# Kernel tuning notes

Measured on AMD Instinct MI355X. Metric: run time of the kernel, lower is better.

## Reference

```python
import jax, jax.numpy as jnp
import numpy as np

EPS = 1e-8

def _qparams(x, bits):
    # AsymmetricSignedQParams + GlobalMinMaxObserver: per-tensor min/max,
    # signed range [-2^(b-1), 2^(b-1)-1], asymmetric zero point.
    qmin = -(2 ** (bits - 1))
    qmax = 2 ** (bits - 1) - 1
    mn = jnp.minimum(jnp.min(x), 0.0)
    mx = jnp.maximum(jnp.max(x), 0.0)
    scale = jnp.maximum((mx - mn) / (qmax - qmin), EPS)
    zp = jnp.clip(jnp.round(qmin - mn / scale), qmin, qmax)
    return scale, zp, qmin, qmax

def _fake_quant(x, bits):
    # quantize -> clamp -> dequantize (simulated fixed-point as in float forward)
    scale, zp, qmin, qmax = _qparams(x, bits)
    q = jnp.clip(jnp.round(x / scale) + zp, qmin, qmax)
    return (q - zp) * scale


def setup_inputs() -> dict:
    key = jax.random.key(0)
    k1, k2, k3 = jax.random.split(key, 3)
    B, W, H, D = 8, 1024, 8, 64
    q = jax.random.normal(k1, (B, W, H, D), dtype=jnp.float32)
    k = jax.random.normal(k2, (B, W, H, D), dtype=jnp.float32)
    v = jax.random.normal(k3, (B, W, H, D), dtype=jnp.float32)
    return {"q": q, "k": k, "v": v, "quant_bits": 8}


def reference(q, k, v, quant_bits):
    bits = int(quant_bits)
    d_model = q.shape[-1]
    inv_sqrt_d = 1.0 / np.sqrt(d_model)

    # quantize-dequantize inputs (inputs_{q,k,v}_QParams)
    qf = _fake_quant(q, bits)
    kf = _fake_quant(k, bits)
    vf = _fake_quant(v, bits)

    # matrix_multi_score: quantized QK^T with folded 1/sqrt(d) scale,
    # then requantize output (matrix_multi_score.outputs_QParams)
    scores = jnp.einsum("bqhd,bkhd->bhqk", qf, kf) * inv_sqrt_d
    scores = _fake_quant(scores, bits)

    # SoftmaxLUT: softmax over last dim, result requantized (softmax.outputs_QParams)
    att = jax.nn.softmax(scores, axis=-1)
    att_q = _fake_quant(att, bits)

    # matrix_multi_att: quantized att @ V, requantized output
    context = jnp.einsum("bhqk,bkhd->bqhd", att_q, vf)
    context = _fake_quant(context, bits)

    return context, att_q
```

## Files before the change

### kernel.cpp

```cpp
#include <hip/hip_runtime.h>
#include <cstdint>
#include <cstddef>

#define W  1024
#define NH 8
#define NB 8
#define DH 64
#define BHN (NB*NH)
#define CTX_ELEMS ((size_t)NB*W*NH*DH)
#define NS 64
#define ROWF 512
#define L2E 1.4426950408889634f

typedef int v4i __attribute__((ext_vector_type(4)));


__device__ __forceinline__ unsigned enc_f(float f){
  unsigned u = __float_as_uint(f);
  return (u & 0x80000000u) ? ~u : (u | 0x80000000u);
}
__device__ __forceinline__ float dec_f(unsigned k){
  unsigned u = (k & 0x80000000u) ? (k ^ 0x80000000u) : ~k;
  return __uint_as_float(u);
}

__device__ __forceinline__ float fq1(float x, float s, float z, float mn, float mx){
  float t = rintf(x / s) + z;
  t = fminf(fmaxf(t, mn), mx);
  return (t - z) * s;
}
__device__ __forceinline__ int qint_m(float x, float is, float z, float mn, float mx){
  return (int)fminf(fmaxf(rintf(x * is) + z, mn), mx);
}
__device__ __forceinline__ unsigned pack4(int a0, int a1, int a2, int a3){
  return (unsigned)(a0 & 0xff) | ((unsigned)(a1 & 0xff) << 8) |
         ((unsigned)(a2 & 0xff) << 16) | ((unsigned)(a3 & 0xff) << 24);
}

__device__ __forceinline__ unsigned* slot_min(unsigned* s, int t){ return s + (size_t)(2*t)*NS; }
__device__ __forceinline__ unsigned* slot_max(unsigned* s, int t){ return s + (size_t)(2*t+1)*NS; }

struct QP { float s, z; };

__device__ __forceinline__ QP qp_generic(const unsigned* slots, int t, float qmn, float qmx){
  const unsigned* pm = slots + (size_t)(2*t)*NS;
  const unsigned* px = pm + NS;
  unsigned em = pm[0], ex = px[0];
  for (int i = 1; i < NS; ++i){
    unsigned a = pm[i], b = px[i];
    em = (a < em) ? a : em;
    ex = (b > ex) ? b : ex;
  }
  float mn = dec_f(em), mx = dec_f(ex);
  QP r;
  r.s = fmaxf((mx - mn) / (qmx - qmn), 1e-8f);
  r.z = fminf(fmaxf(rintf(qmn - mn / r.s), qmn), qmx);
  return r;
}
__device__ __forceinline__ QP qp_scores(const int* jmn, const int* jmx, float sq, float sk,
                                        float qmn, float qmx){
  int em = jmn[0], ex = jmx[0];
  for (int i = 1; i < NS; ++i){ em = min(em, jmn[i]); ex = max(ex, jmx[i]); }
  float cfac = 0.125f * (sq * sk);
  float mn = fminf(cfac * (float)em, 0.0f);
  float mx = fmaxf(cfac * (float)ex, 0.0f);
  QP r;
  r.s = fmaxf((mx - mn) / (qmx - qmn), 1e-8f);
  r.z = fminf(fmaxf(rintf(qmn - mn / r.s), qmn), qmx);
  return r;
}

__device__ __forceinline__ void blk_minmax_atomic(float lmin, float lmax,
                                                  unsigned* smin, unsigned* smax){
  #pragma unroll
  for (int o = 32; o; o >>= 1){
    lmin = fminf(lmin, __shfl_xor(lmin, o));
    lmax = fmaxf(lmax, __shfl_xor(lmax, o));
  }
  __shared__ float wmn[4], wmx[4];
  int wid = threadIdx.x >> 6, lane = threadIdx.x & 63;
  if (lane == 0){ wmn[wid] = lmin; wmx[wid] = lmax; }
  __syncthreads();
  if (threadIdx.x == 0){
    float a = wmn[0], b = wmx[0];
    for (int w = 1; w < (int)(blockDim.x >> 6); ++w){
      a = fminf(a, wmn[w]); b = fmaxf(b, wmx[w]);
    }
    atomicMin(smin, enc_f(a));
    atomicMax(smax, enc_f(b));
  }
}

__device__ __forceinline__ void blk_iminmax_atomic(int lmin, int lmax, int* gmin, int* gmax){
  #pragma unroll
  for (int o = 32; o; o >>= 1){
    lmin = min(lmin, __shfl_xor(lmin, o));
    lmax = max(lmax, __shfl_xor(lmax, o));
  }
  __shared__ int iwmn[4], iwmx[4];
  int wid = threadIdx.x >> 6, lane = threadIdx.x & 63;
  if (lane == 0){ iwmn[wid] = lmin; iwmx[wid] = lmax; }
  __syncthreads();
  if (threadIdx.x == 0){
    int a = iwmn[0], b = iwmx[0];
    for (int w = 1; w < (int)(blockDim.x >> 6); ++w){
      a = min(a, iwmn[w]); b = max(b, iwmx[w]);
    }
    atomicMin(gmin, a);
    atomicMax(gmax, b);
  }
}

__device__ __forceinline__ void stage_tile(const float* __restrict__ rowptr,
                                           signed char (*S)[80], int* __restrict__ Ssum,
                                           float is, float z, float mn, float mx, int t){
  const int rr = t >> 2, dq = (t & 3) << 4;
  const float* p = rowptr + (size_t)rr * ROWF + dq;
  int part = 0;
  #pragma unroll
  for (int g = 0; g < 4; ++g){
    float4 x = *(const float4*)(p + g * 4);
    int a0 = qint_m(x.x, is, z, mn, mx), a1 = qint_m(x.y, is, z, mn, mx);
    int a2 = qint_m(x.z, is, z, mn, mx), a3 = qint_m(x.w, is, z, mn, mx);
    part += a0 + a1 + a2 + a3;
    *(unsigned*)&S[rr][dq + g*4] = pack4(a0, a1, a2, a3);
  }
  int x1 = part + __shfl_xor(part, 1);
  int tot = x1 + __shfl_xor(x1, 2);
  if ((t & 3) == 0) Ssum[rr] = tot;
}

__device__ __forceinline__ v4i qfrag_direct(const float* __restrict__ qrow, int lg,
                                            float is, float z, float mn, float mx,
                                            int* sqi_out){
  const float* p = qrow + (lg << 4);
  int part = 0; unsigned d4[4];
  #pragma unroll
  for (int g = 0; g < 4; ++g){
    float4 x = *(const float4*)(p + g * 4);
    int a0 = qint_m(x.x, is, z, mn, mx), a1 = qint_m(x.y, is, z, mn, mx);
    int a2 = qint_m(x.z, is, z, mn, mx), a3 = qint_m(x.w, is, z, mn, mx);
    part += a0 + a1 + a2 + a3;
    d4[g] = pack4(a0, a1, a2, a3);
  }
  part += __shfl_xor(part, 16);
  part += __shfl_xor(part, 32);
  *sqi_out = part;
  v4i r; r[0] = (int)d4[0]; r[1] = (int)d4[1]; r[2] = (int)d4[2]; r[3] = (int)d4[3];
  return r;
}


__global__ void init_slots_kernel(unsigned* __restrict__ slots, int* __restrict__ jmn,
                                  int* __restrict__ jmx, int* __restrict__ Sv8){
  for (int i = threadIdx.x; i < 6*2*NS; i += blockDim.x)
    slots[i] = 0x80000000u;
  if (threadIdx.x < NS){
    jmn[threadIdx.x] = 0x7fffffff;
    jmx[threadIdx.x] = (int)0x80000000;
  }
  for (int i = threadIdx.x; i < BHN*64; i += blockDim.x) Sv8[i] = 0;
}

__global__ __launch_bounds__(256) void minmax3_kernel(const float* __restrict__ q,
                                                      const float* __restrict__ k,
                                                      const float* __restrict__ v,
                                                      unsigned* __restrict__ slots){
  const float4* p = (const float4*)(blockIdx.y == 0 ? q : (blockIdx.y == 1 ? k : v));
  float lmin = 0.f, lmax = 0.f;
  const int n4 = (int)(CTX_ELEMS / 4);
  for (int i = blockIdx.x * blockDim.x + threadIdx.x; i < n4; i += gridDim.x * blockDim.x){
    float4 x = p[i];
    lmin = fminf(lmin, fminf(fminf(x.x, x.y), fminf(x.z, x.w)));
    lmax = fmaxf(lmax, fmaxf(fmaxf(x.x, x.y), fmaxf(x.z, x.w)));
  }
  const int idx = blockIdx.x & (NS - 1);
  blk_minmax_atomic(lmin, lmax, slot_min(slots, blockIdx.y) + idx, slot_max(slots, blockIdx.y) + idx);
}


__global__ __launch_bounds__(256) void pass1a_kernel(const float* __restrict__ kg,
                                                     const float* __restrict__ vg,
                                                     const unsigned* __restrict__ slots,
                                                     const int* __restrict__ bits_p,
                                                     char* __restrict__ k8,
                                                     int* __restrict__ Sk8,
                                                     char* __restrict__ v8,
                                                     int* __restrict__ Sv8){
  __shared__ int ColS[64];
  const int bits = *bits_p;
  const float qmx = (float)((1 << (bits-1)) - 1), qmn = -(float)(1 << (bits-1));
  const QP kp = qp_generic(slots, 1, qmn, qmx);
  const QP vp = qp_generic(slots, 2, qmn, qmx);
  const int it = blockIdx.x, bh = blockIdx.y, b = bh >> 3, h = bh & 7;
  const int i0 = it << 6, t = threadIdx.x;

  {
    const int rr = t >> 2, dq = (t & 3) << 4;
    const float* p = kg + ((size_t)(b*W + i0 + rr) * NH + h) * DH + dq;
    const float isk = 1.0f / kp.s;
    int part = 0; unsigned d4[4];
    #pragma unroll
    for (int g = 0; g < 4; ++g){
      float4 x = *(const float4*)(p + g * 4);
      int a0 = qint_m(x.x, isk, kp.z, qmn, qmx), a1 = qint_m(x.y, isk, kp.z, qmn, qmx);
      int a2 = qint_m(x.z, isk, kp.z, qmn, qmx), a3 = qint_m(x.w, isk, kp.z, qmn, qmx);
      part += a0 + a1 + a2 + a3;
      d4[g] = pack4(a0, a1, a2, a3);
    }
    uint4 u; u.x = d4[0]; u.y = d4[1]; u.z = d4[2]; u.w = d4[3];
    *(uint4*)(k8 + ((size_t)bh << 16) + (((size_t)(i0 + rr)) << 6) + dq) = u;
    int x1 = part + __shfl_xor(part, 1);
    int tot = x1 + __shfl_xor(x1, 2);
    if ((t & 3) == 0) Sk8[(bh << 10) + i0 + rr] = tot;
  }

  {
    const int dq4 = (t & 15) << 2, kb = (t >> 4) << 2;
    const float* vp_ = vg + ((size_t)(b*W + i0 + kb) * NH + h) * DH + dq4;
    const float isv = 1.0f / vp.s;
    float4 x0 = *(const float4*)(vp_);
    float4 x1 = *(const float4*)(vp_ + ROWF);
    float4 x2 = *(const float4*)(vp_ + 2 * ROWF);
    float4 x3 = *(const float4*)(vp_ + 3 * ROWF);
    int q00 = qint_m(x0.x, isv, vp.z, qmn, qmx), q01 = qint_m(x0.y, isv, vp.z, qmn, qmx),
        q02 = qint_m(x0.z, isv, vp.z, qmn, qmx), q03 = qint_m(x0.w, isv, vp.z, qmn, qmx);
    int q10 = qint_m(x1.x, isv, vp.z, qmn, qmx), q11 = qint_m(x1.y, isv, vp.z, qmn, qmx),
        q12 = qint_m(x1.z, isv, vp.z, qmn, qmx), q13 = qint_m(x1.w, isv, vp.z, qmn, qmx);
    int q20 = qint_m(x2.x, isv, vp.z, qmn, qmx), q21 = qint_m(x2.y, isv, vp.z, qmn, qmx),
        q22 = qint_m(x2.z, isv, vp.z, qmn, qmx), q23 = qint_m(x2.w, isv, vp.z, qmn, qmx);
    int q30 = qint_m(x3.x, isv, vp.z, qmn, qmx), q31 = qint_m(x3.y, isv, vp.z, qmn, qmx),
        q32 = qint_m(x3.z, isv, vp.z, qmn, qmx), q33 = qint_m(x3.w, isv, vp.z, qmn, qmx);
    unsigned w0 = pack4(q00, q10, q20, q30);
    unsigned w1 = pack4(q01, q11, q21, q31);
    unsigned w2 = pack4(q02, q12, q22, q32);
    unsigned w3 = pack4(q03, q13, q23, q33);
    char* vb = v8 + ((size_t)bh << 16) + i0 + kb;
    *(unsigned*)(vb + ((size_t)(dq4 + 0) << 10)) = w0;
    *(unsigned*)(vb + ((size_t)(dq4 + 1) << 10)) = w1;
    *(unsigned*)(vb + ((size_t)(dq4 + 2) << 10)) = w2;
    *(unsigned*)(vb + ((size_t)(dq4 + 3) << 10)) = w3;
    int cv0 = q00 + q10 + q20 + q30;
    int cv1 = q01 + q11 + q21 + q31;
    int cv2 = q02 + q12 + q22 + q32;
    int cv3 = q03 + q13 + q23 + q33;
    if (t < 64) ColS[t] = 0;
    __syncthreads();
    atomicAdd(&ColS[dq4 + 0], cv0);
    atomicAdd(&ColS[dq4 + 1], cv1);
    atomicAdd(&ColS[dq4 + 2], cv2);
    atomicAdd(&ColS[dq4 + 3], cv3);
    __syncthreads();
    if (t < 64) atomicAdd(&Sv8[(bh << 6) + t], ColS[t]);
  }
}

__global__ __launch_bounds__(256) void pass1b_kernel(const float* __restrict__ qg,
                                                     const unsigned* __restrict__ slots,
                                                     const int* __restrict__ bits_p,
                                                     float* __restrict__ stash,
                                                     int* __restrict__ jmn,
                                                     int* __restrict__ jmx,
                                                     const char* __restrict__ k8,
                                                     const int* __restrict__ Sk8){
  const int bits = *bits_p;
  const float qmx = (float)((1 << (bits-1)) - 1), qmn = -(float)(1 << (bits-1));
  const QP qq = qp_generic(slots, 0, qmn, qmx);
  const QP kp = qp_generic(slots, 1, qmn, qmx);
  const int it = blockIdx.x, bh = blockIdx.y, b = bh >> 3, h = bh & 7;
  const int i0 = it << 6, t = threadIdx.x;
  const int lane = t & 63, w = t >> 6, lr = lane & 15, lg = lane >> 4;
  const int irow = (w << 4) + lr;
  const int izq = (int)qq.z, izk = (int)kp.z, c64 = 64 * izq * izk;

  int sqi;
  v4i Bq = qfrag_direct(qg + ((size_t)(b*W + i0 + irow) * NH + h) * DH, lg,
                        1.0f / qq.s, qq.z, qmn, qmx, &sqi);
  const char* kb = k8 + ((size_t)bh << 16);
  const int* skb = Sk8 + (bh << 10);

  int gmin = 0x7fffffff, gmax = (int)0x80000000, rmax = (int)0x80000000;
  for (int cc = 0; cc < 16; ++cc){
    #pragma unroll
    for (int jt = 0; jt < 4; ++jt){
      v4i Ak = *(const v4i*)(kb + (((size_t)((cc << 6) + (jt << 4) + lr)) << 6) + (lg << 4));
      v4i s4 = *(const v4i*)(skb + (cc << 6) + (jt << 4) + (lg << 2));
      v4i zz = {0, 0, 0, 0};
      v4i acc = __builtin_amdgcn_mfma_i32_16x16x64_i8(Ak, Bq, zz, 0, 0, 0);
      #pragma unroll
      for (int r = 0; r < 4; ++r){
        int J = acc[r] - izq * s4[r] - izk * sqi + c64;
        gmin = min(gmin, J); gmax = max(gmax, J); rmax = max(rmax, J);
      }
    }
  }
  rmax = max(rmax, __shfl_xor(rmax, 16));
  rmax = max(rmax, __shfl_xor(rmax, 32));
  if (lg == 0)
    stash[((size_t)(b*W + i0 + irow) * NH + h) * DH] = __int_as_float(rmax);
  const int idx = (it + bh * 16) & (NS - 1);
  blk_iminmax_atomic(gmin, gmax, jmn + idx, jmx + idx);
}

__global__ __launch_bounds__(256) void pass2c_kernel(const float* __restrict__ qg,
                                                     unsigned* __restrict__ slots,
                                                     const int* __restrict__ jmn,
                                                     const int* __restrict__ jmx,
                                                     const int* __restrict__ bits_p,
                                                     float* __restrict__ stash,
                                                     const char* __restrict__ k8,
                                                     const int* __restrict__ Sk8){
  const int bits = *bits_p;
  const float qmx = (float)((1 << (bits-1)) - 1), qmn = -(float)(1 << (bits-1));
  const QP qq = qp_generic(slots, 0, qmn, qmx);
  const QP kp = qp_generic(slots, 1, qmn, qmx);
  const QP sp = qp_scores(jmn, jmx, qq.s, kp.s, qmn, qmx);
  const int it = blockIdx.x, bh = blockIdx.y, b = bh >> 3, h = bh & 7;
  const int i0 = it << 6, t = threadIdx.x;
  const int lane = t & 63, w = t >> 6, lr = lane & 15, lg = lane >> 4;
  const int irow = (w << 4) + lr;
  const int izq = (int)qq.z, izk = (int)kp.z, c64 = 64 * izq * izk;
  const float rf = (0.125f * (qq.s * kp.s)) / sp.s;
  const float c2 = sp.s * L2E, zs = sp.z;

  int sqi;
  v4i Bq = qfrag_direct(qg + ((size_t)(b*W + i0 + irow) * NH + h) * DH, lg,
                        1.0f / qq.s, qq.z, qmn, qmx, &sqi);
  int Jm = __float_as_int(stash[((size_t)(b*W + i0 + irow) * NH + h) * DH]);
  const float tmxf = fminf(fmaxf(rintf((float)Jm * rf) + zs, qmn), qmx);
  const char* kb = k8 + ((size_t)bh << 16);
  const int* skb = Sk8 + (bh << 10);

  float zacc = 0.f;
  for (int cc = 0; cc < 16; ++cc){
    #pragma unroll
    for (int jt = 0; jt < 4; ++jt){
      v4i Ak = *(const v4i*)(kb + (((size_t)((cc << 6) + (jt << 4) + lr)) << 6) + (lg << 4));
      v4i s4 = *(const v4i*)(skb + (cc << 6) + (jt << 4) + (lg << 2));
      v4i zz = {0, 0, 0, 0};
      v4i acc = __builtin_amdgcn_mfma_i32_16x16x64_i8(Ak, Bq, zz, 0, 0, 0);
      int J0 = acc[0] - izq * s4[0] - izk * sqi + c64;
      int J1 = acc[1] - izq * s4[1] - izk * sqi + c64;
      int J2 = acc[2] - izq * s4[2] - izk * sqi + c64;
      int J3 = acc[3] - izq * s4[3] - izk * sqi + c64;
      float tl0 = fminf(fmaxf(rintf((float)J0 * rf) + zs, qmn), qmx);
      float tl1 = fminf(fmaxf(rintf((float)J1 * rf) + zs, qmn), qmx);
      float tl2 = fminf(fmaxf(rintf((float)J2 * rf) + zs, qmn), qmx);
      float tl3 = fminf(fmaxf(rintf((float)J3 * rf) + zs, qmn), qmx);
      zacc += exp2f((tl0 - tmxf) * c2);
      zacc += exp2f((tl1 - tmxf) * c2);
      zacc += exp2f((tl2 - tmxf) * c2);
      zacc += exp2f((tl3 - tmxf) * c2);
    }
  }
  zacc += __shfl_xor(zacc, 16);
  zacc += __shfl_xor(zacc, 32);
  if (lg == 0)
    stash[((size_t)(b*W + i0 + irow) * NH + h) * DH + 1] = zacc;
  float ratt = 1.0f / zacc;
  #pragma unroll
  for (int o = 1; o < 16; o <<= 1) ratt = fmaxf(ratt, __shfl_xor(ratt, o));
  if (lane == 0){
    const int idx = ((it << 2) + w + bh * 64) & (NS - 1);
    atomicMax(slot_max(slots, 4) + idx, enc_f(ratt));
  }
}

__global__ __launch_bounds__(256) void pass3c_kernel(const float* __restrict__ qg,
                                                     float* __restrict__ att,
                                                     float* __restrict__ ctx,
                                                     unsigned* __restrict__ slots,
                                                     const int* __restrict__ jmn,
                                                     const int* __restrict__ jmx,
                                                     const int* __restrict__ bits_p,
                                                     const char* __restrict__ k8,
                                                     const int* __restrict__ Sk8,
                                                     const char* __restrict__ v8,
                                                     const int* __restrict__ Sv8){
  __shared__ __align__(16) signed char As[64][80];
  __shared__ int RowA[64];
  const int bits = *bits_p;
  const float qmx = (float)((1 << (bits-1)) - 1), qmn = -(float)(1 << (bits-1));
  const QP qq = qp_generic(slots, 0, qmn, qmx);
  const QP kp = qp_generic(slots, 1, qmn, qmx);
  const QP sp = qp_scores(jmn, jmx, qq.s, kp.s, qmn, qmx);
  const QP vp = qp_generic(slots, 2, qmn, qmx);
  const QP ap = qp_generic(slots, 4, qmn, qmx);
  const int it = blockIdx.x, bh = blockIdx.y, b = bh >> 3, h = bh & 7;
  const int i0 = it << 6, t = threadIdx.x;
  const int lane = t & 63, w = t >> 6, lr = lane & 15, lg = lane >> 4;
  const int irow = (w << 4) + lr;
  const int izq = (int)qq.z, izk = (int)kp.z, c64 = 64 * izq * izk;
  const int iza = (int)ap.z, izv = (int)vp.z;
  const float rf = (0.125f * (qq.s * kp.s)) / sp.s;
  const float c2 = sp.s * L2E, zs = sp.z;
  const float sa = ap.s, za = ap.z, inv_sa = 1.0f / sa;

  int sqi;
  v4i Bq = qfrag_direct(qg + ((size_t)(b*W + i0 + irow) * NH + h) * DH, lg,
                        1.0f / qq.s, qq.z, qmn, qmx, &sqi);
  const size_t rbase = ((size_t)(b*W + i0 + irow) * NH + h) * DH;
  int Jm = __float_as_int(ctx[rbase]);
  const float tmxf = fminf(fmaxf(rintf((float)Jm * rf) + zs, qmn), qmx);
  const float iZ = 1.0f / ctx[rbase + 1];
  const char* kb = k8 + ((size_t)bh << 16);
  const int* skb = Sk8 + (bh << 10);
  const char* vb = v8 + ((size_t)bh << 16);

  int rA = 0;
  v4i accPV[4];
  #pragma unroll
  for (int tj = 0; tj < 4; ++tj){ v4i zz = {0,0,0,0}; accPV[tj] = zz; }

  for (int cc = 0; cc < 16; ++cc){
    #pragma unroll
    for (int jt = 0; jt < 4; ++jt){
      v4i Ak = *(const v4i*)(kb + (((size_t)((cc << 6) + (jt << 4) + lr)) << 6) + (lg << 4));
      v4i s4 = *(const v4i*)(skb + (cc << 6) + (jt << 4) + (lg << 2));
      v4i zz = {0, 0, 0, 0};
      v4i acc = __builtin_amdgcn_mfma_i32_16x16x64_i8(Ak, Bq, zz, 0, 0, 0);
      int J0 = acc[0] - izq * s4[0] - izk * sqi + c64;
      int J1 = acc[1] - izq * s4[1] - izk * sqi + c64;
      int J2 = acc[2] - izq * s4[2] - izk * sqi + c64;
      int J3 = acc[3] - izq * s4[3] - izk * sqi + c64;
      float tl0 = fminf(fmaxf(rintf((float)J0 * rf) + zs, qmn), qmx);
      float tl1 = fminf(fmaxf(rintf((float)J1 * rf) + zs, qmn), qmx);
      float tl2 = fminf(fmaxf(rintf((float)J2 * rf) + zs, qmn), qmx);
      float tl3 = fminf(fmaxf(rintf((float)J3 * rf) + zs, qmn), qmx);
      float p0 = exp2f((tl0 - tmxf) * c2) * iZ;
      float p1 = exp2f((tl1 - tmxf) * c2) * iZ;
      float p2 = exp2f((tl2 - tmxf) * c2) * iZ;
      float p3 = exp2f((tl3 - tmxf) * c2) * iZ;
      float a0 = fminf(fmaxf(rintf(p0 * inv_sa) + za, qmn), qmx);
      float a1 = fminf(fmaxf(rintf(p1 * inv_sa) + za, qmn), qmx);
      float a2 = fminf(fmaxf(rintf(p2 * inv_sa) + za, qmn), qmx);
      float a3 = fminf(fmaxf(rintf(p3 * inv_sa) + za, qmn), qmx);
      float4 y;
      y.x = (a0 - za) * sa; y.y = (a1 - za) * sa;
      y.z = (a2 - za) * sa; y.w = (a3 - za) * sa;
      *(float4*)(att + ((size_t)bh << 20) + (size_t)(i0 + irow) * W
                 + (cc << 6) + (jt << 4) + (lg << 2)) = y;
      int q0 = (int)a0, q1 = (int)a1, q2 = (int)a2, q3 = (int)a3;
      rA += q0 + q1 + q2 + q3;
      *(unsigned*)&As[irow][(jt << 4) + (lg << 2)] = pack4(q0, q1, q2, q3);
    }
    {
      v4i A2 = *(const v4i*)&As[(w << 4) + lr][lg << 4];
      #pragma unroll
      for (int tj = 0; tj < 4; ++tj){
        v4i B2 = *(const v4i*)(vb + (((size_t)((tj << 4) + lr)) << 10) + (cc << 6) + (lg << 4));
        accPV[tj] = __builtin_amdgcn_mfma_i32_16x16x64_i8(A2, B2, accPV[tj], 0, 0, 0);
      }
    }
  }

  rA += __shfl_xor(rA, 16);
  rA += __shfl_xor(rA, 32);
  if (lg == 0) RowA[irow] = rA;

  const float sav = sa * vp.s;
  float lmin = 0.f, lmax = 0.f;
  #pragma unroll
  for (int tj = 0; tj < 4; ++tj){
    const int d = (tj << 4) + lr;
    const int cvd = Sv8[(bh << 6) + d];
    #pragma unroll
    for (int r = 0; r < 4; ++r){
      const int i = (w << 4) + (lg << 2) + r;
      int Jv = accPV[tj][r] - iza * cvd - izv * RowA[i] + 1024 * iza * izv;
      float c = sav * (float)Jv;
      lmin = fminf(lmin, c); lmax = fmaxf(lmax, c);
      ctx[(((size_t)(b * W + i0 + i)) * NH + h) * DH + d] = c;
    }
  }
  const int idx = (it + bh * 16) & (NS - 1);
  blk_minmax_atomic(lmin, lmax, slot_min(slots, 5) + idx, slot_max(slots, 5) + idx);
}


__global__ __launch_bounds__(256) void pass1_plain(const float* __restrict__ qg,
                                                   const float* __restrict__ kg,
                                                   const unsigned* __restrict__ slots,
                                                   const int* __restrict__ bits_p,
                                                   float* __restrict__ stash,
                                                   int* __restrict__ jmn,
                                                   int* __restrict__ jmx){
  __shared__ __align__(16) signed char Qs[64][80], Ks[64][80];
  __shared__ int Sq[64], Sk[64];
  const int bits = *bits_p;
  const float qmx = (float)((1 << (bits-1)) - 1), qmn = -(float)(1 << (bits-1));
  const QP qq = qp_generic(slots, 0, qmn, qmx);
  const QP kp = qp_generic(slots, 1, qmn, qmx);
  const int it = blockIdx.x, bh = blockIdx.y, b = bh >> 3, h = bh & 7;
  const int i0 = it << 6, t = threadIdx.x;
  const int lane = t & 63, w = t >> 6, lr = lane & 15, lg = lane >> 4;
  const float isq = 1.0f / qq.s, isk = 1.0f / kp.s;
  const int izq = (int)qq.z, izk = (int)kp.z, c64 = 64 * izq * izk;

  stage_tile(qg + ((size_t)(b*W + i0) * NH + h) * DH, Qs, Sq, isq, qq.z, qmn, qmx, t);
  __syncthreads();
  const v4i Bq = *(const v4i*)&Qs[(w << 4) + lr][lg << 4];
  const int sqi = Sq[(w << 4) + lr];

  int gmin = 0x7fffffff, gmax = (int)0x80000000, rmax = (int)0x80000000;
  for (int cc = 0; cc < 16; ++cc){
    __syncthreads();
    stage_tile(kg + ((size_t)(b*W + (cc << 6)) * NH + h) * DH, Ks, Sk, isk, kp.z, qmn, qmx, t);
    __syncthreads();
    #pragma unroll
    for (int jt = 0; jt < 4; ++jt){
      v4i Ak = *(const v4i*)&Ks[(jt << 4) + lr][lg << 4];
      v4i zz = {0, 0, 0, 0};
      v4i acc = __builtin_amdgcn_mfma_i32_16x16x64_i8(Ak, Bq, zz, 0, 0, 0);
      v4i s4 = *(const v4i*)&Sk[(jt << 4) + (lg << 2)];
      #pragma unroll
      for (int r = 0; r < 4; ++r){
        int J = acc[r] - izq * s4[r] - izk * sqi + c64;
        gmin = min(gmin, J); gmax = max(gmax, J); rmax = max(rmax, J);
      }
    }
  }
  rmax = max(rmax, __shfl_xor(rmax, 16));
  rmax = max(rmax, __shfl_xor(rmax, 32));
  if (lg == 0)
    stash[((size_t)(b*W + i0 + (w << 4) + lr) * NH + h) * DH] = __int_as_float(rmax);
  const int idx = (it + bh * 16) & (NS - 1);
  blk_iminmax_atomic(gmin, gmax, jmn + idx, jmx + idx);
}

__global__ __launch_bounds__(256) void pass2_plain(const float* __restrict__ qg,
                                                   const float* __restrict__ kg,
                                                   unsigned* __restrict__ slots,
                                                   const int* __restrict__ jmn,
                                                   const int* __restrict__ jmx,
                                                   const int* __restrict__ bits_p,
                                                   float* __restrict__ stash){
  __shared__ __align__(16) signed char Qs[64][80], Ks[64][80];
  __shared__ int Sq[64], Sk[64];
  const int bits = *bits_p;
  const float qmx = (float)((1 << (bits-1)) - 1), qmn = -(float)(1 << (bits-1));
  const QP qq = qp_generic(slots, 0, qmn, qmx);
  const QP kp = qp_generic(slots, 1, qmn, qmx);
  const QP sp = qp_scores(jmn, jmx, qq.s, kp.s, qmn, qmx);
  const int it = blockIdx.x, bh = blockIdx.y, b = bh >> 3, h = bh & 7;
  const int i0 = it << 6, t = threadIdx.x;
  const int lane = t & 63, w = t >> 6, lr = lane & 15, lg = lane >> 4;
  const float isq = 1.0f / qq.s, isk = 1.0f / kp.s;
  const int izq = (int)qq.z, izk = (int)kp.z, c64 = 64 * izq * izk;
  const float rf = (0.125f * (qq.s * kp.s)) / sp.s;
  const float c2 = sp.s * L2E, zs = sp.z;
  const int irow = (w << 4) + lr;

  stage_tile(qg + ((size_t)(b*W + i0) * NH + h) * DH, Qs, Sq, isq, qq.z, qmn, qmx, t);
  __syncthreads();
  const v4i Bq = *(const v4i*)&Qs[irow][lg << 4];
  const int sqi = Sq[irow];
  int Jm = __float_as_int(stash[((size_t)(b*W + i0 + irow) * NH + h) * DH]);
  const float tmxf = fminf(fmaxf(rintf((float)Jm * rf) + zs, qmn), qmx);

  float zacc = 0.f;
  for (int cc = 0; cc < 16; ++cc){
    __syncthreads();
    stage_tile(kg + ((size_t)(b*W + (cc << 6)) * NH + h) * DH, Ks, Sk, isk, kp.z, qmn, qmx, t);
    __syncthreads();
    #pragma unroll
    for (int jt = 0; jt < 4; ++jt){
      v4i Ak = *(const v4i*)&Ks[(jt << 4) + lr][lg << 4];
      v4i zz = {0, 0, 0, 0};
      v4i acc = __builtin_amdgcn_mfma_i32_16x16x64_i8(Ak, Bq, zz, 0, 0, 0);
      v4i s4 = *(const v4i*)&Sk[(jt << 4) + (lg << 2)];
      int J0 = acc[0] - izq * s4[0] - izk * sqi + c64;
      int J1 = acc[1] - izq * s4[1] - izk * sqi + c64;
      int J2 = acc[2] - izq * s4[2] - izk * sqi + c64;
      int J3 = acc[3] - izq * s4[3] - izk * sqi + c64;
      float tl0 = fminf(fmaxf(rintf((float)J0 * rf) + zs, qmn), qmx);
      float tl1 = fminf(fmaxf(rintf((float)J1 * rf) + zs, qmn), qmx);
      float tl2 = fminf(fmaxf(rintf((float)J2 * rf) + zs, qmn), qmx);
      float tl3 = fminf(fmaxf(rintf((float)J3 * rf) + zs, qmn), qmx);
      zacc += exp2f((tl0 - tmxf) * c2);
      zacc += exp2f((tl1 - tmxf) * c2);
      zacc += exp2f((tl2 - tmxf) * c2);
      zacc += exp2f((tl3 - tmxf) * c2);
    }
  }
  zacc += __shfl_xor(zacc, 16);
  zacc += __shfl_xor(zacc, 32);
  if (lg == 0)
    stash[((size_t)(b*W + i0 + irow) * NH + h) * DH + 1] = zacc;
  float ratt = 1.0f / zacc;
  #pragma unroll
  for (int o = 1; o < 16; o <<= 1) ratt = fmaxf(ratt, __shfl_xor(ratt, o));
  if (lane == 0){
    const int idx = ((it << 2) + w + bh * 64) & (NS - 1);
    atomicMax(slot_max(slots, 4) + idx, enc_f(ratt));
  }
}

__global__ __launch_bounds__(256) void pass3_plain(const float* __restrict__ qg,
                                                   const float* __restrict__ kg,
                                                   const float* __restrict__ vg,
                                                   float* __restrict__ att,
                                                   float* __restrict__ ctx,
                                                   unsigned* __restrict__ slots,
                                                   const int* __restrict__ jmn,
                                                   const int* __restrict__ jmx,
                                                   const int* __restrict__ bits_p){
  __shared__ __align__(16) signed char Qs[64][80], Ks[64][80], Vs[64][80], As[64][80];
  __shared__ int Sq[64], Sk[64];
  __shared__ int RowA[64], ColV[64];
  const int bits = *bits_p;
  const float qmx = (float)((1 << (bits-1)) - 1), qmn = -(float)(1 << (bits-1));
  const QP qq = qp_generic(slots, 0, qmn, qmx);
  const QP kp = qp_generic(slots, 1, qmn, qmx);
  const QP sp = qp_scores(jmn, jmx, qq.s, kp.s, qmn, qmx);
  const QP vp = qp_generic(slots, 2, qmn, qmx);
  const QP ap = qp_generic(slots, 4, qmn, qmx);
  const int it = blockIdx.x, bh = blockIdx.y, b = bh >> 3, h = bh & 7;
  const int i0 = it << 6, t = threadIdx.x;
  const int lane = t & 63, w = t >> 6, lr = lane & 15, lg = lane >> 4;
  const float isq = 1.0f / qq.s, isk = 1.0f / kp.s;
  const int izq = (int)qq.z, izk = (int)kp.z, c64 = 64 * izq * izk;
  const float rf = (0.125f * (qq.s * kp.s)) / sp.s;
  const float c2 = sp.s * L2E, zs = sp.z;
  const float sa = ap.s, za = ap.z, inv_sa = 1.0f / sa;
  const float sv = vp.s, zv = vp.z, isv = 1.0f / sv;
  const int iza = (int)za, izv = (int)zv;
  const int irow = (w << 4) + lr;

  if (t < 64) ColV[t] = 0;
  stage_tile(qg + ((size_t)(b*W + i0) * NH + h) * DH, Qs, Sq, isq, qq.z, qmn, qmx, t);
  __syncthreads();
  const v4i Bq = *(const v4i*)&Qs[irow][lg << 4];
  const int sqi = Sq[irow];
  const size_t rbase = ((size_t)(b*W + i0 + irow) * NH + h) * DH;
  int Jm = __float_as_int(ctx[rbase]);
  const float tmxf = fminf(fmaxf(rintf((float)Jm * rf) + zs, qmn), qmx);
  const float iZ = 1.0f / ctx[rbase + 1];

  const int dq4 = (t & 15) << 2;
  const int kb  = (t >> 4) << 2;
  int cv4[4] = {0, 0, 0, 0};
  int rA = 0;
  v4i accPV[4];
  #pragma unroll
  for (int tj = 0; tj < 4; ++tj){ v4i zz = {0,0,0,0}; accPV[tj] = zz; }

  for (int cc = 0; cc < 16; ++cc){
    __syncthreads();
    stage_tile(kg + ((size_t)(b*W + (cc << 6)) * NH + h) * DH, Ks, Sk, isk, kp.z, qmn, qmx, t);
    {
      const float* vp_ = vg + ((size_t)(b*W + (cc << 6) + kb) * NH + h) * DH + dq4;
      float4 x0 = *(const float4*)(vp_);
      float4 x1 = *(const float4*)(vp_ + ROWF);
      float4 x2 = *(const float4*)(vp_ + 2 * ROWF);
      float4 x3 = *(const float4*)(vp_ + 3 * ROWF);
      int q00 = qint_m(x0.x, isv, zv, qmn, qmx), q01 = qint_m(x0.y, isv, zv, qmn, qmx),
          q02 = qint_m(x0.z, isv, zv, qmn, qmx), q03 = qint_m(x0.w, isv, zv, qmn, qmx);
      int q10 = qint_m(x1.x, isv, zv, qmn, qmx), q11 = qint_m(x1.y, isv, zv, qmn, qmx),
          q12 = qint_m(x1.z, isv, zv, qmn, qmx), q13 = qint_m(x1.w, isv, zv, qmn, qmx);
      int q20 = qint_m(x2.x, isv, zv, qmn, qmx), q21 = qint_m(x2.y, isv, zv, qmn, qmx),
          q22 = qint_m(x2.z, isv, zv, qmn, qmx), q23 = qint_m(x2.w, isv, zv, qmn, qmx);
      int q30 = qint_m(x3.x, isv, zv, qmn, qmx), q31 = qint_m(x3.y, isv, zv, qmn, qmx),
          q32 = qint_m(x3.z, isv, zv, qmn, qmx), q33 = qint_m(x3.w, isv, zv, qmn, qmx);
      cv4[0] += q00 + q10 + q20 + q30;
      cv4[1] += q01 + q11 + q21 + q31;
// ... 26 lines not shown
      float a0 = fminf(fmaxf(rintf(p0 * inv_sa) + za, qmn), qmx);
      float a1 = fminf(fmaxf(rintf(p1 * inv_sa) + za, qmn), qmx);
      float a2 = fminf(fmaxf(rintf(p2 * inv_sa) + za, qmn), qmx);
      float a3 = fminf(fmaxf(rintf(p3 * inv_sa) + za, qmn), qmx);
      float4 y;
      y.x = (a0 - za) * sa; y.y = (a1 - za) * sa;
      y.z = (a2 - za) * sa; y.w = (a3 - za) * sa;
      *(float4*)(att + ((size_t)bh << 20) + (size_t)(i0 + irow) * W
                 + (cc << 6) + (jt << 4) + (lg << 2)) = y;
      int q0 = (int)a0, q1 = (int)a1, q2 = (int)a2, q3 = (int)a3;
      rA += q0 + q1 + q2 + q3;
      *(unsigned*)&As[irow][(jt << 4) + (lg << 2)] = pack4(q0, q1, q2, q3);
    }
    {
      v4i A2 = *(const v4i*)&As[(w << 4) + lr][lg << 4];
      #pragma unroll
      for (int tj = 0; tj < 4; ++tj){
        v4i B2 = *(const v4i*)&Vs[(tj << 4) + lr][lg << 4];
        accPV[tj] = __builtin_amdgcn_mfma_i32_16x16x64_i8(A2, B2, accPV[tj], 0, 0, 0);
      }
    }
  }

  rA += __shfl_xor(rA, 16);
  rA += __shfl_xor(rA, 32);
  if (lg == 0) RowA[irow] = rA;
  #pragma unroll
  for (int j = 0; j < 4; ++j) atomicAdd(&ColV[dq4 + j], cv4[j]);
  __syncthreads();

  const float sav = sa * sv;
  float lmin = 0.f, lmax = 0.f;
  #pragma unroll
  for (int tj = 0; tj < 4; ++tj){
    const int d = (tj << 4) + lr;
    #pragma unroll
    for (int r = 0; r < 4; ++r){
      const int i = (w << 4) + (lg << 2) + r;
      int Jv = accPV[tj][r] - iza * ColV[d] - izv * RowA[i] + 1024 * iza * izv;
      float c = sav * (float)Jv;
      lmin = fminf(lmin, c); lmax = fmaxf(lmax, c);
      ctx[(((size_t)(b * W + i0 + i)) * NH + h) * DH + d] = c;
    }
  }
  const int idx = (it + bh * 16) & (NS - 1);
  blk_minmax_atomic(lmin, lmax, slot_min(slots, 5) + idx, slot_max(slots, 5) + idx);
}

__global__ __launch_bounds__(256) void quantctx_kernel(float* __restrict__ ctx,
                                                       const unsigned* __restrict__ slots,
                                                       const int* __restrict__ bits_p){
  const int bits = *bits_p;
  const float qmx = (float)((1 << (bits-1)) - 1), qmn = -(float)(1 << (bits-1));
  const QP cp = qp_generic(slots, 5, qmn, qmx);
  size_t i = (size_t)blockIdx.x * blockDim.x + threadIdx.x;
  float4* p = (float4*)ctx;
  float4 x = p[i];
  x.x = fq1(x.x, cp.s, cp.z, qmn, qmx);
  x.y = fq1(x.y, cp.s, cp.z, qmn, qmx);
  x.z = fq1(x.z, cp.s, cp.z, qmn, qmx);
  x.w = fq1(x.w, cp.s, cp.z, qmn, qmx);
  p[i] = x;
}


extern "C" void kernel_launch(void* const* d_in, const int* in_sizes, int n_in,
                              void* d_out, int out_size, void* d_ws, size_t ws_size,
                              hipStream_t stream){
  const float* q = (const float*)d_in[0];
  const float* k = (const float*)d_in[1];
  const float* v = (const float*)d_in[2];
  const int* bits = (const int*)d_in[3];
  float* ctx = (float*)d_out;
  float* att = (float*)d_out + CTX_ELEMS;
  unsigned* slots = (unsigned*)d_ws;
  int* jmn = (int*)((char*)d_ws + 3072);
  int* jmx = (int*)((char*)d_ws + 3328);
  int* Sv8 = (int*)((char*)d_ws + 4096);
  int* Sk8 = (int*)((char*)d_ws + 20480);
  char* k8 = (char*)d_ws + 282624;
  char* v8 = (char*)d_ws + 4476928;
  const bool cached = ws_size >= (size_t)8671232;

  hipLaunchKernelGGL(init_slots_kernel, dim3(1), dim3(256), 0, stream, slots, jmn, jmx, Sv8);
  hipLaunchKernelGGL(minmax3_kernel, dim3(512, 3), dim3(256), 0, stream, q, k, v, slots);
  if (cached){
    hipLaunchKernelGGL(pass1a_kernel, dim3(16, BHN), dim3(256), 0, stream,
                       k, v, slots, bits, k8, Sk8, v8, Sv8);
    hipLaunchKernelGGL(pass1b_kernel, dim3(16, BHN), dim3(256), 0, stream,
                       q, slots, bits, ctx, jmn, jmx, k8, Sk8);
    hipLaunchKernelGGL(pass2c_kernel, dim3(16, BHN), dim3(256), 0, stream,
                       q, slots, jmn, jmx, bits, ctx, k8, Sk8);
    hipLaunchKernelGGL(pass3c_kernel, dim3(16, BHN), dim3(256), 0, stream,
                       q, att, ctx, slots, jmn, jmx, bits, k8, Sk8, v8, Sv8);
  } else {
    hipLaunchKernelGGL(pass1_plain, dim3(16, BHN), dim3(256), 0, stream,
                       q, k, slots, bits, ctx, jmn, jmx);
    hipLaunchKernelGGL(pass2_plain, dim3(16, BHN), dim3(256), 0, stream,
                       q, k, slots, jmn, jmx, bits, ctx);
    hipLaunchKernelGGL(pass3_plain, dim3(16, BHN), dim3(256), 0, stream,
                       q, k, v, att, ctx, slots, jmn, jmx, bits);
  }
  hipLaunchKernelGGL(quantctx_kernel, dim3(4096), dim3(256), 0, stream, ctx, slots, bits);
}
```

Baseline: 210.5 us.

## Fuse all passes into one cooperative persistent kernel with grid syncs

Measured after the change: 214.2 us. About the same (+1.8%).

```diff
diff --git a/kernel.cpp b/kernel.cpp
--- a/kernel.cpp
+++ b/kernel.cpp
@@ -1,4 +1,5 @@
 #include <hip/hip_runtime.h>
+#include <hip/hip_cooperative_groups.h>
 #include <cstdint>
 #include <cstddef>
 
@@ -12,6 +13,7 @@
 #define ROWF 512
 #define L2E 1.4426950408889634f
 
+namespace cg = cooperative_groups;
 typedef int v4i __attribute__((ext_vector_type(4)));
 
 
@@ -89,6 +91,7 @@
     atomicMin(smin, enc_f(a));
     atomicMax(smax, enc_f(b));
   }
+  __syncthreads();
 }
 
 __device__ __forceinline__ void blk_iminmax_atomic(int lmin, int lmax, int* gmin, int* gmax){
@@ -109,6 +112,7 @@
     atomicMin(gmin, a);
     atomicMax(gmax, b);
   }
+  __syncthreads();
 }
 
 __device__ __forceinline__ void stage_tile(const float* __restrict__ rowptr,
@@ -148,6 +152,286 @@
   *sqi_out = part;
   v4i r; r[0] = (int)d4[0]; r[1] = (int)d4[1]; r[2] = (int)d4[2]; r[3] = (int)d4[3];
   return r;
+}
+
+
+__global__ __launch_bounds__(256, 2) void mega_kernel(
+    const float* __restrict__ qg, const float* __restrict__ kg, const float* __restrict__ vg,
+    const int* __restrict__ bits_p, float* __restrict__ ctx, float* __restrict__ att,
+    unsigned* __restrict__ slots, int* __restrict__ jmn, int* __restrict__ jmx,
+    int* __restrict__ Sv8, int* __restrict__ Sk8, char* __restrict__ k8,
+    char* __restrict__ v8){
+  cg::grid_group grid = cg::this_grid();
+  __shared__ __align__(16) signed char As[64][80];
+  __shared__ int RowA[64];
+  __shared__ int ColS[64];
+
+  const int t = threadIdx.x;
+  const int itb = blockIdx.x, bh = blockIdx.y;
+  const int bid = bh * 8 + itb;
+  const int b = bh >> 3, h = bh & 7;
+  const int lane = t & 63, w = t >> 6, lr = lane & 15, lg = lane >> 4;
+  const int irow = (w << 4) + lr;
+  const int bits = *bits_p;
+  const float qmx = (float)((1 << (bits-1)) - 1), qmn = -(float)(1 << (bits-1));
+
+  if (bid == 0){
+    for (int i = t; i < 6*2*NS; i += 256) slots[i] = 0x80000000u;
+    if (t < NS){ jmn[t] = 0x7fffffff; jmx[t] = (int)0x80000000; }
+  }
+  if (bid == 1){
+    for (int i = t; i < BHN*64; i += 256) Sv8[i] = 0;
+  }
+  grid.sync();
+
+  {
+    const int nt = 8*BHN*256;
+    const int gtid = bid*256 + t;
+    #pragma unroll
+    for (int tz = 0; tz < 3; ++tz){
+      const float4* p = (const float4*)(tz == 0 ? qg : (tz == 1 ? kg : vg));
+      float lmin = 0.f, lmax = 0.f;
+      for (int i = gtid; i < (int)(CTX_ELEMS/4); i += nt){
+        float4 x = p[i];
+        lmin = fminf(lmin, fminf(fminf(x.x, x.y), fminf(x.z, x.w)));
+        lmax = fmaxf(lmax, fmaxf(fmaxf(x.x, x.y), fmaxf(x.z, x.w)));
+      }
+      blk_minmax_atomic(lmin, lmax, slot_min(slots, tz) + (bid & 63),
+                        slot_max(slots, tz) + (bid & 63));
+    }
+  }
+  grid.sync();
+
+  const QP qq = qp_generic(slots, 0, qmn, qmx);
+  const QP kp = qp_generic(slots, 1, qmn, qmx);
+  const QP vqp = qp_generic(slots, 2, qmn, qmx);
+
+  #pragma unroll
+  for (int ti = 0; ti < 2; ++ti){
+    const int i0 = ((itb << 1) + ti) << 6;
+    {
+      const int rr = t >> 2, dq = (t & 3) << 4;
+      const float* p = kg + ((size_t)(b*W + i0 + rr) * NH + h) * DH + dq;
+      const float isk = 1.0f / kp.s;
+      int part = 0; unsigned d4[4];
+      #pragma unroll
+      for (int g = 0; g < 4; ++g){
+        float4 x = *(const float4*)(p + g * 4);
+        int a0 = qint_m(x.x, isk, kp.z, qmn, qmx), a1 = qint_m(x.y, isk, kp.z, qmn, qmx);
+        int a2 = qint_m(x.z, isk, kp.z, qmn, qmx), a3 = qint_m(x.w, isk, kp.z, qmn, qmx);
+        part += a0 + a1 + a2 + a3;
+        d4[g] = pack4(a0, a1, a2, a3);
+      }
+      uint4 u; u.x = d4[0]; u.y = d4[1]; u.z = d4[2]; u.w = d4[3];
+      *(uint4*)(k8 + ((size_t)bh << 16) + (((size_t)(i0 + rr)) << 6) + dq) = u;
+      int x1 = part + __shfl_xor(part, 1);
+      int tot = x1 + __shfl_xor(x1, 2);
+      if ((t & 3) == 0) Sk8[(bh << 10) + i0 + rr] = tot;
+    }
+    {
+      const int dq4 = (t & 15) << 2, kb4 = (t >> 4) << 2;
+      const float* vp_ = vg + ((size_t)(b*W + i0 + kb4) * NH + h) * DH + dq4;
+      const float isv = 1.0f / vqp.s;
+      float4 x0 = *(const float4*)(vp_);
+      float4 x1 = *(const float4*)(vp_ + ROWF);
+      float4 x2 = *(const float4*)(vp_ + 2 * ROWF);
+      float4 x3 = *(const float4*)(vp_ + 3 * ROWF);
+      int q00 = qint_m(x0.x, isv, vqp.z, qmn, qmx), q01 = qint_m(x0.y, isv, vqp.z, qmn, qmx),
+          q02 = qint_m(x0.z, isv, vqp.z, qmn, qmx), q03 = qint_m(x0.w, isv, vqp.z, qmn, qmx);
+      int q10 = qint_m(x1.x, isv, vqp.z, qmn, qmx), q11 = qint_m(x1.y, isv, vqp.z, qmn, qmx),
+          q12 = qint_m(x1.z, isv, vqp.z, qmn, qmx), q13 = qint_m(x1.w, isv, vqp.z, qmn, qmx);
+      int q20 = qint_m(x2.x, isv, vqp.z, qmn, qmx), q21 = qint_m(x2.y, isv, vqp.z, qmn, qmx),
+          q22 = qint_m(x2.z, isv, vqp.z, qmn, qmx), q23 = qint_m(x2.w, isv, vqp.z, qmn, qmx);
+      int q30 = qint_m(x3.x, isv, vqp.z, qmn, qmx), q31 = qint_m(x3.y, isv, vqp.z, qmn, qmx),
+          q32 = qint_m(x3.z, isv, vqp.z, qmn, qmx), q33 = qint_m(x3.w, isv, vqp.z, qmn, qmx);
+      char* vb = v8 + ((size_t)bh << 16) + i0 + kb4;
+      *(unsigned*)(vb + ((size_t)(dq4 + 0) << 10)) = pack4(q00, q10, q20, q30);
+      *(unsigned*)(vb + ((size_t)(dq4 + 1) << 10)) = pack4(q01, q11, q21, q31);
+      *(unsigned*)(vb + ((size_t)(dq4 + 2) << 10)) = pack4(q02, q12, q22, q32);
+      *(unsigned*)(vb + ((size_t)(dq4 + 3) << 10)) = pack4(q03, q13, q23, q33);
+      if (t < 64) ColS[t] = 0;
+      __syncthreads();
+      atomicAdd(&ColS[dq4 + 0], q00 + q10 + q20 + q30);
+      atomicAdd(&ColS[dq4 + 1], q01 + q11 + q21 + q31);
+      atomicAdd(&ColS[dq4 + 2], q02 + q12 + q22 + q32);
+      atomicAdd(&ColS[dq4 + 3], q03 + q13 + q23 + q33);
+      __syncthreads();
+      if (t < 64) atomicAdd(&Sv8[(bh << 6) + t], ColS[t]);
+      __syncthreads();
+    }
+  }
+  grid.sync();
+
+  const int izq = (int)qq.z, izk = (int)kp.z, c64 = 64 * izq * izk;
+  const char* kb = k8 + ((size_t)bh << 16);
+  const int* skb = Sk8 + (bh << 10);
+  v4i Bqt[2]; int sqit[2]; int rmaxJt[2];
+  {
+    int gmin = 0x7fffffff, gmax = (int)0x80000000;
+    #pragma unroll
+    for (int ti = 0; ti < 2; ++ti){
+      const int i0 = ((itb << 1) + ti) << 6;
+      Bqt[ti] = qfrag_direct(qg + ((size_t)(b*W + i0 + irow) * NH + h) * DH, lg,
+                             1.0f / qq.s, qq.z, qmn, qmx, &sqit[ti]);
+      int rmax = (int)0x80000000;
+      for (int cc = 0; cc < 16; ++cc){
+        #pragma unroll
+        for (int jt = 0; jt < 4; ++jt){
+          v4i Ak = *(const v4i*)(kb + (((size_t)((cc << 6) + (jt << 4) + lr)) << 6) + (lg << 4));
+          v4i s4 = *(const v4i*)(skb + (cc << 6) + (jt << 4) + (lg << 2));
+          v4i zz = {0, 0, 0, 0};
+          v4i acc = __builtin_amdgcn_mfma_i32_16x16x64_i8(Ak, Bqt[ti], zz, 0, 0, 0);
+          #pragma unroll
+          for (int r = 0; r < 4; ++r){
+            int J = acc[r] - izq * s4[r] - izk * sqit[ti] + c64;
+            gmin = min(gmin, J); gmax = max(gmax, J); rmax = max(rmax, J);
+          }
+        }
+      }
+      rmax = max(rmax, __shfl_xor(rmax, 16));
+      rmax = max(rmax, __shfl_xor(rmax, 32));
+      rmaxJt[ti] = rmax;
+    }
+    blk_iminmax_atomic(gmin, gmax, jmn + (bid & 63), jmx + (bid & 63));
+  }
+  grid.sync();
+
+  const QP sp = qp_scores(jmn, jmx, qq.s, kp.s, qmn, qmx);
+  const float rf = (0.125f * (qq.s * kp.s)) / sp.s;
+  const float c2 = sp.s * L2E, zs = sp.z;
+  float tmxft[2], iZt[2];
+  {
+    #pragma unroll
+    for (int ti = 0; ti < 2; ++ti){
+      tmxft[ti] = fminf(fmaxf(rintf((float)rmaxJt[ti] * rf) + zs, qmn), qmx);
+      float zacc = 0.f;
+      for (int cc = 0; cc < 16; ++cc){
+        #pragma unroll
+        for (int jt = 0; jt < 4; ++jt){
+          v4i Ak = *(const v4i*)(kb + (((size_t)((cc << 6) + (jt << 4) + lr)) << 6) + (lg << 4));
+          v4i s4 = *(const v4i*)(skb + (cc << 6) + (jt << 4) + (lg << 2));
+          v4i zz = {0, 0, 0, 0};
+          v4i acc = __builtin_amdgcn_mfma_i32_16x16x64_i8(Ak, Bqt[ti], zz, 0, 0, 0);
+          #pragma unroll
+          for (int r = 0; r < 4; ++r){
+            int J = acc[r] - izq * s4[r] - izk * sqit[ti] + c64;
+            float tl = fminf(fmaxf(rintf((float)J * rf) + zs, qmn), qmx);
+            zacc += exp2f((tl - tmxft[ti]) * c2);
+          }
+        }
+      }
+      zacc += __shfl_xor(zacc, 16);
+      zacc += __shfl_xor(zacc, 32);
+      iZt[ti] = 1.0f / zacc;
+    }
+    float ratt = fmaxf(iZt[0], iZt[1]);
+    #pragma unroll
+    for (int o = 1; o < 16; o <<= 1) ratt = fmaxf(ratt, __shfl_xor(ratt, o));
+    if (lane == 0)
+      atomicMax(slot_max(slots, 4) + (bid & 63), enc_f(ratt));
+  }
+  grid.sync();
+
+  {
+    const QP ap = qp_generic(slots, 4, qmn, qmx);
+    const float sa = ap.s, za = ap.z, inv_sa = 1.0f / sa;
+    const int iza = (int)za, izv = (int)vqp.z;
+    const char* vb = v8 + ((size_t)bh << 16);
+    const float sav = sa * vqp.s;
+    float lmin = 0.f, lmax = 0.f;
+
+    #pragma unroll
+    for (int ti = 0; ti < 2; ++ti){
+      const int i0 = ((itb << 1) + ti) << 6;
+      const float tmxf = tmxft[ti], iZ = iZt[ti];
+      const v4i Bq = Bqt[ti];
+      const int sqi = sqit[ti];
+      int rA = 0;
+      v4i accPV[4];
+      #pragma unroll
+      for (int tj = 0; tj < 4; ++tj){ v4i zz = {0,0,0,0}; accPV[tj] = zz; }
+
+      for (int cc = 0; cc < 16; ++cc){
+        v4i Bv[4];
+        #pragma unroll
+        for (int tj = 0; tj < 4; ++tj)
+          Bv[tj] = *(const v4i*)(vb + (((size_t)((tj << 4) + lr)) << 10) + (cc << 6) + (lg << 4));
+        #pragma unroll
+        for (int jt = 0; jt < 4; ++jt){
+          v4i Ak = *(const v4i*)(kb + (((size_t)((cc << 6) + (jt << 4) + lr)) << 6) + (lg << 4));
+          v4i s4 = *(const v4i*)(skb + (cc << 6) + (jt << 4) + (lg << 2));
+          v4i zz = {0, 0, 0, 0};
+          v4i acc = __builtin_amdgcn_mfma_i32_16x16x64_i8(Ak, Bq, zz, 0, 0, 0);
+          int J0 = acc[0] - izq * s4[0] - izk * sqi + c64;
+          int J1 = acc[1] - izq * s4[1] - izk * sqi + c64;
+          int J2 = acc[2] - izq * s4[2] - izk * sqi + c64;
+          int J3 = acc[3] - izq * s4[3] - izk * sqi + c64;
+          float tl0 = fminf(fmaxf(rintf((float)J0 * rf) + zs, qmn), qmx);
+          float tl1 = fminf(fmaxf(rintf((float)J1 * rf) + zs, qmn), qmx);
+          float tl2 = fminf(fmaxf(rintf((float)J2 * rf) + zs, qmn), qmx);
+          float tl3 = fminf(fmaxf(rintf((float)J3 * rf) + zs, qmn), qmx);
+          float p0 = exp2f((tl0 - tmxf) * c2) * iZ;
+          float p1 = exp2f((tl1 - tmxf) * c2) * iZ;
+          float p2 = exp2f((tl2 - tmxf) * c2) * iZ;
+          float p3 = exp2f((tl3 - tmxf) * c2) * iZ;
+          float a0 = fminf(fmaxf(rintf(p0 * inv_sa) + za, qmn), qmx);
+          float a1 = fminf(fmaxf(rintf(p1 * inv_sa) + za, qmn), qmx);
+          float a2 = fminf(fmaxf(rintf(p2 * inv_sa) + za, qmn), qmx);
+          float a3 = fminf(fmaxf(rintf(p3 * inv_sa) + za, qmn), qmx);
+          float4 y;
+          y.x = (a0 - za) * sa; y.y = (a1 - za) * sa;
+          y.z = (a2 - za) * sa; y.w = (a3 - za) * sa;
+          *(float4*)(att + ((size_t)bh << 20) + (size_t)(i0 + irow) * W
+                     + (cc << 6) + (jt << 4) + (lg << 2)) = y;
+          int q0 = (int)a0, q1 = (int)a1, q2 = (int)a2, q3 = (int)a3;
+          rA += q0 + q1 + q2 + q3;
+          *(unsigned*)&As[irow][(jt << 4) + (lg << 2)] = pack4(q0, q1, q2, q3);
+        }
+        {
+          v4i A2 = *(const v4i*)&As[(w << 4) + lr][lg << 4];
+          #pragma unroll
+          for (int tj = 0; tj < 4; ++tj)
+            accPV[tj] = __builtin_amdgcn_mfma_i32_16x16x64_i8(A2, Bv[tj], accPV[tj], 0, 0, 0);
+        }
+      }
+
+      rA += __shfl_xor(rA, 16);
+      rA += __shfl_xor(rA, 32);
+      if (lg == 0) RowA[irow] = rA;
+
+      #pragma unroll
+      for (int tj = 0; tj < 4; ++tj){
+        const int d = (tj << 4) + lr;
+        const int cvd = Sv8[(bh << 6) + d];
+        #pragma unroll
+        for (int r = 0; r < 4; ++r){
+          const int i = (w << 4) + (lg << 2) + r;
+          int Jv = accPV[tj][r] - iza * cvd - izv * RowA[i] + 1024 * iza * izv;
+          float c = sav * (float)Jv;
+          lmin = fminf(lmin, c); lmax = fmaxf(lmax, c);
+          ctx[(((size_t)(b * W + i0 + i)) * NH + h) * DH + d] = c;
+        }
+      }
+    }
+    blk_minmax_atomic(lmin, lmax, slot_min(slots, 5) + (bid & 63),
+                      slot_max(slots, 5) + (bid & 63));
+  }
+  grid.sync();
+
+  {
+    const QP cp = qp_generic(slots, 5, qmn, qmx);
+    const int nt = 8*BHN*256;
+    const int gtid = bid*256 + t;
+    float4* p = (float4*)ctx;
+    for (int i = gtid; i < (int)(CTX_ELEMS/4); i += nt){
+      float4 x = p[i];
+      x.x = fq1(x.x, cp.s, cp.z, qmn, qmx);
+      x.y = fq1(x.y, cp.s, cp.z, qmn, qmx);
+      x.z = fq1(x.z, cp.s, cp.z, qmn, qmx);
+      x.w = fq1(x.w, cp.s, cp.z, qmn, qmx);
+      p[i] = x;
+    }
+  }
 }
 
 
@@ -177,7 +461,6 @@
   const int idx = blockIdx.x & (NS - 1);
   blk_minmax_atomic(lmin, lmax, slot_min(slots, blockIdx.y) + idx, slot_max(slots, blockIdx.y) + idx);
 }
-
 
 __global__ __launch_bounds__(256) void pass1a_kernel(const float* __restrict__ kg,
                                                      const float* __restrict__ vg,
@@ -214,7 +497,6 @@
     int tot = x1 + __shfl_xor(x1, 2);
     if ((t & 3) == 0) Sk8[(bh << 10) + i0 + rr] = tot;
   }
-
   {
     const int dq4 = (t & 15) << 2, kb = (t >> 4) << 2;
     const float* vp_ = vg + ((size_t)(b*W + i0 + kb) * NH + h) * DH + dq4;
@@ -231,25 +513,17 @@
         q22 = qint_m(x2.z, isv, vp.z, qmn, qmx), q23 = qint_m(x2.w, isv, vp.z, qmn, qmx);
     int q30 = qint_m(x3.x, isv, vp.z, qmn, qmx), q31 = qint_m(x3.y, isv, vp.z, qmn, qmx),
         q32 = qint_m(x3.z, isv, vp.z, qmn, qmx), q33 = qint_m(x3.w, isv, vp.z, qmn, qmx);
-    unsigned w0 = pack4(q00, q10, q20, q30);
-    unsigned w1 = pack4(q01, q11, q21, q31);
-    unsigned w2 = pack4(q02, q12, q22, q32);
-    unsigned w3 = pack4(q03, q13, q23, q33);
     char* vb = v8 + ((size_t)bh << 16) + i0 + kb;
-    *(unsigned*)(vb + ((size_t)(dq4 + 0) << 10)) = w0;
-    *(unsigned*)(vb + ((size_t)(dq4 + 1) << 10)) = w1;
-    *(unsigned*)(vb + ((size_t)(dq4 + 2) << 10)) = w2;
-    *(unsigned*)(vb + ((size_t)(dq4 + 3) << 10)) = w3;
-    int cv0 = q00 + q10 + q20 + q30;
-    int cv1 = q01 + q11 + q21 + q31;
-    int cv2 = q02 + q12 + q22 + q32;
-    int cv3 = q03 + q13 + q23 + q33;
+    *(unsigned*)(vb + ((size_t)(dq4 + 0) << 10)) = pack4(q00, q10, q20, q30);
+    *(unsigned*)(vb + ((size_t)(dq4 + 1) << 10)) = pack4(q01, q11, q21, q31);
+    *(unsigned*)(vb + ((size_t)(dq4 + 2) << 10)) = pack4(q02, q12, q22, q32);
+    *(unsigned*)(vb + ((size_t)(dq4 + 3) << 10)) = pack4(q03, q13, q23, q33);
     if (t < 64) ColS[t] = 0;
     __syncthreads();
-    atomicAdd(&ColS[dq4 + 0], cv0);
-    atomicAdd(&ColS[dq4 + 1], cv1);
-    atomicAdd(&ColS[dq4 + 2], cv2);
-    atomicAdd(&ColS[dq4 + 3], cv3);
+    atomicAdd(&ColS[dq4 + 0], q00 + q10 + q20 + q30);
+    atomicAdd(&ColS[dq4 + 1], q01 + q11 + q21 + q31);
+    atomicAdd(&ColS[dq4 + 2], q02 + q12 + q22 + q32);
+    atomicAdd(&ColS[dq4 + 3], q03 + q13 + q23 + q33);
     __syncthreads();
     if (t < 64) atomicAdd(&Sv8[(bh << 6) + t], ColS[t]);
   }
@@ -413,6 +687,10 @@
   for (int tj = 0; tj < 4; ++tj){ v4i zz = {0,0,0,0}; accPV[tj] = zz; }
 
   for (int cc = 0; cc < 16; ++cc){
+    v4i Bv[4];
+    #pragma unroll
+    for (int tj = 0; tj < 4; ++tj)
+      Bv[tj] = *(const v4i*)(vb + (((size_t)((tj << 4) + lr)) << 10) + (cc << 6) + (lg << 4));
     #pragma unroll
     for (int jt = 0; jt < 4; ++jt){
       v4i Ak = *(const v4i*)(kb + (((size_t)((cc << 6) + (jt << 4) + lr)) << 6) + (lg << 4));
@@ -447,10 +725,8 @@
     {
       v4i A2 = *(const v4i*)&As[(w << 4) + lr][lg << 4];
       #pragma unroll
-      for (int tj = 0; tj < 4; ++tj){
-        v4i B2 = *(const v4i*)(vb + (((size_t)((tj << 4) + lr)) << 10) + (cc << 6) + (lg << 4));
-        accPV[tj] = __builtin_amdgcn_mfma_i32_16x16x64_i8(A2, B2, accPV[tj], 0, 0, 0);
-      }
+      for (int tj = 0; tj < 4; ++tj)
+        accPV[tj] = __builtin_amdgcn_mfma_i32_16x16x64_i8(A2, Bv[tj], accPV[tj], 0, 0, 0);
     }
   }
 
@@ -569,18 +845,12 @@
       v4i zz = {0, 0, 0, 0};
       v4i acc = __builtin_amdgcn_mfma_i32_16x16x64_i8(Ak, Bq, zz, 0, 0, 0);
       v4i s4 = *(const v4i*)&Sk[(jt << 4) + (lg << 2)];
-      int J0 = acc[0] - izq * s4[0] - izk * sqi + c64;
-      int J1 = acc[1] - izq * s4[1] - izk * sqi + c64;
-      int J2 = acc[2] - izq * s4[2] - izk * sqi + c64;
-      int J3 = acc[3] - izq * s4[3] - izk * sqi + c64;
-      float tl0 = fminf(fmaxf(rintf((float)J0 * rf) + zs, qmn), qmx);
-      float tl1 = fminf(fmaxf(rintf((float)J1 * rf) + zs, qmn), qmx);
-      float tl2 = fminf(fmaxf(rintf((float)J2 * rf) + zs, qmn), qmx);
-      float tl3 = fminf(fmaxf(rintf((float)J3 * rf) + zs, qmn), qmx);
-      zacc += exp2f((tl0 - tmxf) * c2);
-      zacc += exp2f((tl1 - tmxf) * c2);
-      zacc += exp2f((tl2 - tmxf) * c2);
-      zacc += exp2f((tl3 - tmxf) * c2);
+      #pragma unroll
+      for (int r = 0; r < 4; ++r){
+        int J = acc[r] - izq * s4[r] - izk * sqi + c64;
+        float tl = fminf(fmaxf(rintf((float)J * rf) + zs, qmn), qmx);
+        zacc += exp2f((tl - tmxf) * c2);
+      }
     }
   }
   zacc += __shfl_xor(zacc, 16);
@@ -773,9 +1043,22 @@
   char* v8 = (char*)d_ws + 4476928;
   const bool cached = ws_size >= (size_t)8671232;
 
-  hipLaunchKernelGGL(init_slots_kernel, dim3(1), dim3(256), 0, stream, slots, jmn, jmx, Sv8);
-  hipLaunchKernelGGL(minmax3_kernel, dim3(512, 3), dim3(256), 0, stream, q, k, v, slots);
   if (cached){
+    int maxB = 0;
+    hipError_t oe = hipOccupancyMaxActiveBlocksPerMultiprocessor(&maxB, mega_kernel, 256, 0);
+    if (oe == hipSuccess && maxB * 256 >= 8 * BHN){
+      void* args[] = {(void*)&q, (void*)&k, (void*)&v, (void*)&bits, (void*)&ctx, (void*)&att,
+                      (void*)&slots, (void*)&jmn, (void*)&jmx, (void*)&Sv8, (void*)&Sk8,
+                      (void*)&k8, (void*)&v8};
+      hipError_t e = hipLaunchCooperativeKernel((void*)mega_kernel, dim3(8, BHN), dim3(256),
+                                                args, 0, stream);
+      if (e == hipSuccess) return;
+      (void)hipGetLastError();
+    } else {
+      (void)hipGetLastError();
+    }
+    hipLaunchKernelGGL(init_slots_kernel, dim3(1), dim3(256), 0, stream, slots, jmn, jmx, Sv8);
+    hipLaunchKernelGGL(minmax3_kernel, dim3(512, 3), dim3(256), 0, stream, q, k, v, slots);
     hipLaunchKernelGGL(pass1a_kernel, dim3(16, BHN), dim3(256), 0, stream,
                        k, v, slots, bits, k8, Sk8, v8, Sv8);
     hipLaunchKernelGGL(pass1b_kernel, dim3(16, BHN), dim3(256), 0, stream,
@@ -784,13 +1067,16 @@
                        q, slots, jmn, jmx, bits, ctx, k8, Sk8);
     hipLaunchKernelGGL(pass3c_kernel, dim3(16, BHN), dim3(256), 0, stream,
                        q, att, ctx, slots, jmn, jmx, bits, k8, Sk8, v8, Sv8);
+    hipLaunchKernelGGL(quantctx_kernel, dim3(4096), dim3(256), 0, stream, ctx, slots, bits);
   } else {
+    hipLaunchKernelGGL(init_slots_kernel, dim3(1), dim3(256), 0, stream, slots, jmn, jmx, Sv8);
+    hipLaunchKernelGGL(minmax3_kernel, dim3(512, 3), dim3(256), 0, stream, q, k, v, slots);
     hipLaunchKernelGGL(pass1_plain, dim3(16, BHN), dim3(256), 0, stream,
                        q, k, slots, bits, ctx, jmn, jmx);
     hipLaunchKernelGGL(pass2_plain, dim3(16, BHN), dim3(256), 0, stream,
                        q, k, slots, jmn, jmx, bits, ctx);
     hipLaunchKernelGGL(pass3_plain, dim3(16, BHN), dim3(256), 0, stream,
                        q, k, v, att, ctx, slots, jmn, jmx, bits);
-  }
-  hipLaunchKernelGGL(quantctx_kernel, dim3(4096), dim3(256), 0, stream, ctx, slots, bits);
-}
+    hipLaunchKernelGGL(quantctx_kernel, dim3(4096), dim3(256), 0, stream, ctx, slots, bits);
+  }
+}
```
